# Kernel tuning notes

Measured on AMD Instinct MI355X. Metric: run time of the kernel, lower is better.

The kernel has to match this reference:

```python
import jax, jax.numpy as jnp
import numpy as np

EPS_STD = 1e-5   # PNA std aggregator epsilon
EPS_GN = 1e-5    # GraphNorm epsilon


def setup_inputs() -> dict:
    key = jax.random.key(0)
    B, N, C = 8, 256, 128
    ks = jax.random.split(key, 8)
    w = lambda k, sh: jax.random.normal(k, sh, jnp.float32) * 0.05
    return {
        "x": jax.random.normal(ks[0], (B, N, C), jnp.float32),
        "edge": jax.random.normal(ks[1], (B, N * N, C), jnp.float32),
        "W_edge": w(ks[2], (C, C)), "b_edge": jnp.zeros((C,), jnp.float32),
        "W_pre": w(ks[3], (3 * C, C)), "b_pre": jnp.zeros((C,), jnp.float32),
        "W_post": w(ks[4], (5 * C, C)), "b_post": jnp.zeros((C,), jnp.float32),
        "W_lin": w(ks[5], (C, C)), "b_lin": jnp.zeros((C,), jnp.float32),
        "gn_weight": jnp.ones((C,), jnp.float32),
        "gn_bias": jnp.zeros((C,), jnp.float32),
        "gn_alpha": jnp.ones((C,), jnp.float32),
    }


def reference(x, edge, W_edge, b_edge, W_pre, b_pre, W_post, b_post,
              W_lin, b_lin, gn_weight, gn_bias, gn_alpha):
    B, N, C = x.shape
    res = x
    # edge e = i*N + j: source j -> target i  => reshape to [B, i(target), j(source), C]
    e = edge.reshape(B, N, N, C)
    e_enc = e @ W_edge + b_edge                               # edge_encoder
    x_i = jnp.broadcast_to(x[:, :, None, :], (B, N, N, C))    # target feats
    x_j = jnp.broadcast_to(x[:, None, :, :], (B, N, N, C))    # source feats
    h = jnp.concatenate([x_i, x_j, e_enc], axis=-1)           # [B,N,N,3C]
    m = h @ W_pre + b_pre                                     # pre-MLP messages [B,N,N,C]
    # PNA aggregators over source axis j (graph is fully connected, degree == N)
    mean = m.mean(axis=2)
    mn = m.min(axis=2)
    mx = m.max(axis=2)
    var = (m * m).mean(axis=2) - mean * mean
    std = jnp.sqrt(jax.nn.relu(var) + EPS_STD)
    agg = jnp.concatenate([mean, mn, mx, std], axis=-1)       # [B,N,4C]
    out = jnp.concatenate([x, agg], axis=-1) @ W_post + b_post  # post-MLP [B,N,C]
    out = out @ W_lin + b_lin                                  # final linear
    # GraphNorm with batch=None in the original: stats over ALL B*N nodes
    flat = out.reshape(B * N, C)
    mu = flat.mean(axis=0, keepdims=True)
    centered = flat - gn_alpha * mu
    v = (centered * centered).mean(axis=0, keepdims=True)
    normed = gn_weight * centered / jnp.sqrt(v + EPS_GN) + gn_bias
    y = jax.nn.relu(normed).reshape(B, N, C)
    return y + res
```

## Files before the change

### kernel.cpp

```cpp
#include <hip/hip_runtime.h>
#include <hip/hip_bf16.h>
#include <stdint.h>

typedef __attribute__((ext_vector_type(8))) short bf16x8;
typedef __attribute__((ext_vector_type(4))) float f32x4;
typedef __attribute__((ext_vector_type(4))) unsigned int u32x4;

#define NB 256
#define CC 128

typedef const __attribute__((address_space(1))) void* gvp;
typedef __attribute__((address_space(3))) void* lvp;
#define GLOAD_LDS16(GP, LP) \
  __builtin_amdgcn_global_load_lds((gvp)(uintptr_t)(GP), (lvp)(uintptr_t)(LP), 16, 0, 0)

static __device__ __forceinline__ unsigned int cvt_pk_bf16(float lo, float hi) {
  unsigned int r;
  asm("v_cvt_pk_bf16_f32 %0, %1, %2" : "=v"(r) : "v"(lo), "v"(hi));
  return r;
}
static __device__ __forceinline__ uint16_t f2bf(float f) {
  unsigned u = __builtin_bit_cast(unsigned, f);
  return (uint16_t)((u + 0x7FFFu + ((u >> 16) & 1u)) >> 16);
}

__global__ void k_prep(const float* __restrict__ W_edge, const float* __restrict__ b_edge,
                       const float* __restrict__ W_pre, const float* __restrict__ b_pre,
                       const float* __restrict__ x,
                       uint16_t* __restrict__ wct, float* __restrict__ bc2,
                       float* __restrict__ At, float* __restrict__ Bv) {
  const int c = threadIdx.x;
  if (blockIdx.x < 128) {
    const int k = blockIdx.x;
    float acc = 0.f;
    for (int q = 0; q < CC; ++q)
      acc += W_edge[k * CC + q] * W_pre[(2 * CC + q) * CC + c];
    wct[c * CC + k] = f2bf(acc);
    if (k == 0) {
      float a2 = b_pre[c];
      for (int q = 0; q < CC; ++q) a2 += b_edge[q] * W_pre[(2 * CC + q) * CC + c];
      bc2[c] = a2;
    }
  } else {
    const int m0 = (blockIdx.x - 128) * 2;
    __shared__ float xs[2][CC];
    xs[0][c] = x[(size_t)m0 * CC + c];
    xs[1][c] = x[(size_t)(m0 + 1) * CC + c];
    __syncthreads();
    float a0 = 0.f, a1 = 0.f, v0 = 0.f, v1 = 0.f;
#pragma unroll 4
    for (int k = 0; k < CC; ++k) {
      const float w1 = W_pre[k * CC + c];
      const float w2 = W_pre[(CC + k) * CC + c];
      a0 += xs[0][k] * w1; a1 += xs[1][k] * w1;
      v0 += xs[0][k] * w2; v1 += xs[1][k] * w2;
    }
    At[(size_t)m0 * CC + c] = a0;       At[(size_t)(m0 + 1) * CC + c] = a1;
    Bv[(size_t)m0 * CC + c] = v0;       Bv[(size_t)(m0 + 1) * CC + c] = v1;
  }
}

__global__ __launch_bounds__(256, 4) void k_edge(
    const float* __restrict__ edge, const uint16_t* __restrict__ wct,
    const float* __restrict__ Bv, const float* __restrict__ At,
    const float* __restrict__ bc2, float* __restrict__ agg) {
  __shared__ __align__(16) float ebuf[3][2048];
  __shared__ __align__(16) float bvbuf[2][2048];

  const int blk  = blockIdx.x;
  const int b    = blk >> 8;
  const int tid  = threadIdx.x;
  const int lane = tid & 63;
  const int wv   = tid >> 6;
  const int g    = lane >> 4;
  const int lr   = lane & 15;
  const int cb   = wv * 32;

  bf16x8 bfr[2][4];
#pragma unroll
  for (int t = 0; t < 2; ++t) {
    const uint16_t* p1 = wct + (cb + t * 16 + lr) * CC + g * 8;
#pragma unroll
    for (int ks = 0; ks < 4; ++ks)
      bfr[t][ks] = *(const bf16x8*)(p1 + ks * 32);
  }
  asm volatile("s_waitcnt vmcnt(0)" ::: "memory");

  const uint32_t L0 = wv * 2048 + lane * 16;
  const uint32_t L1 = L0 + 1024;
  const uint32_t S0 = L0 ^ (((L0 >> 9) & 7) << 4);
  const uint32_t S1 = L1 ^ (((L1 >> 9) & 7) << 4);

  const char* egbase  = (const char*)(edge + (size_t)blk * (NB * CC));
  const char* bvgbase = (const char*)(Bv + (size_t)b * (NB * CC));

  auto STAGE_E = [&](int buf, int t) {
    const char* eg = egbase + (size_t)t * 8192;
    char* el = (char*)&ebuf[buf][0];
    GLOAD_LDS16(eg + S0, el + wv * 2048);
    GLOAD_LDS16(eg + S1, el + wv * 2048 + 1024);
  };
  auto STAGE_BV = [&](int buf, int t) {
    const char* bg = bvgbase + (size_t)t * 8192;
    char* bl = (char*)&bvbuf[buf][0];
    GLOAD_LDS16(bg + S0, bl + wv * 2048);
    GLOAD_LDS16(bg + S1, bl + wv * 2048 + 1024);
  };

  float sum0 = 0.f, sum1 = 0.f, ssq0 = 0.f, ssq1 = 0.f;
  float mn0 = 1e30f, mn1 = 1e30f, mx0 = -1e30f, mx1 = -1e30f;
  const int swz = (lr & 7) << 4;

  auto COMPUTE = [&](int ebi, int bvi) {
    const char* eb = (const char*)&ebuf[ebi][0] + lr * 512;
    const char* bb = (const char*)&bvbuf[bvi][0];
    f32x4 acc0 = {0.f, 0.f, 0.f, 0.f}, acc1 = {0.f, 0.f, 0.f, 0.f};
#pragma unroll
    for (int ks = 0; ks < 4; ++ks) {
      const int off = g * 32 + ks * 128;
      f32x4 lo = *(const f32x4*)(eb + (off ^ swz));
      f32x4 hi = *(const f32x4*)(eb + ((off + 16) ^ swz));
      u32x4 aw;
      aw.x = cvt_pk_bf16(lo.x, lo.y);
      aw.y = cvt_pk_bf16(lo.z, lo.w);
      aw.z = cvt_pk_bf16(hi.x, hi.y);
      aw.w = cvt_pk_bf16(hi.z, hi.w);
      bf16x8 af = __builtin_bit_cast(bf16x8, aw);
      acc0 = __builtin_amdgcn_mfma_f32_16x16x32_bf16(af, bfr[0][ks], acc0, 0, 0, 0);
      acc1 = __builtin_amdgcn_mfma_f32_16x16x32_bf16(af, bfr[1][ks], acc1, 0, 0, 0);
    }
#pragma unroll
    for (int r = 0; r < 4; ++r) {
      const int row = g * 4 + r;
      const int sw = (row & 7) << 4;
      const int lin0 = row * 512 + (cb + lr) * 4;
      const float bv0 = *(const float*)(bb + (lin0 ^ sw));
      const float bv1 = *(const float*)(bb + ((lin0 + 64) ^ sw));
      float s0 = acc0[r] + bv0;
      float s1 = acc1[r] + bv1;
      sum0 += s0; ssq0 = fmaf(s0, s0, ssq0);
      mn0 = fminf(mn0, s0); mx0 = fmaxf(mx0, s0);
      sum1 += s1; ssq1 = fmaf(s1, s1, ssq1);
      mn1 = fminf(mn1, s1); mx1 = fmaxf(mx1, s1);
    }
  };

  STAGE_E(0, 0); STAGE_BV(0, 0); STAGE_E(1, 1);

  int eu = 0;
  int bu = 0;
#pragma unroll 1
  for (int t = 0; t < 14; ++t) {
    asm volatile("s_waitcnt vmcnt(2)" ::: "memory");
    __builtin_amdgcn_s_barrier();
    __builtin_amdgcn_sched_barrier(0);
    int esb = eu - 1; if (esb < 0) esb = 2;
    STAGE_BV(bu ^ 1, t + 1);
    STAGE_E(esb, t + 2);
    __builtin_amdgcn_sched_barrier(0);
    COMPUTE(eu, bu);
    eu = (eu == 2) ? 0 : eu + 1;
    bu ^= 1;
  }
  asm volatile("s_waitcnt vmcnt(2)" ::: "memory");
  __builtin_amdgcn_s_barrier();
  __builtin_amdgcn_sched_barrier(0);
  STAGE_BV(1, 15);
  __builtin_amdgcn_sched_barrier(0);
  COMPUTE(2, 0);
  asm volatile("s_waitcnt vmcnt(0)" ::: "memory");
  __builtin_amdgcn_s_barrier();
  __builtin_amdgcn_sched_barrier(0);
  COMPUTE(0, 1);

#pragma unroll
  for (int m = 16; m <= 32; m <<= 1) {
    sum0 += __shfl_xor(sum0, m); ssq0 += __shfl_xor(ssq0, m);
    mn0 = fminf(mn0, __shfl_xor(mn0, m)); mx0 = fmaxf(mx0, __shfl_xor(mx0, m));
    sum1 += __shfl_xor(sum1, m); ssq1 += __shfl_xor(ssq1, m);
    mn1 = fminf(mn1, __shfl_xor(mn1, m)); mx1 = fmaxf(mx1, __shfl_xor(mx1, m));
  }
  if (g == 0) {
#pragma unroll
    for (int t = 0; t < 2; ++t) {
      const int col = cb + t * 16 + lr;
      const float s   = t ? sum1 : sum0;
      const float q   = t ? ssq1 : ssq0;
      const float mnv = t ? mn1 : mn0;
      const float mxv = t ? mx1 : mx0;
      const float tt = At[blk * CC + col] + bc2[col];
      const float mean = s * (1.f / NB);
      const float var = q * (1.f / NB) - mean * mean;
      const float sd = sqrtf(fmaxf(var, 0.f) + 1e-5f);
      float* ap = agg + (size_t)blk * (4 * CC) + col;
      ap[0]      = tt + mean;
      ap[CC]     = tt + mnv;
      ap[2 * CC] = tt + mxv;
      ap[3 * CC] = sd;
    }
  }
}

__global__ __launch_bounds__(256) void k_post(
    const float* __restrict__ x, const float* __restrict__ agg,
    const float* __restrict__ W_post, const float* __restrict__ b_post,
    const float* __restrict__ W_lin, const float* __restrict__ b_lin,
    float* __restrict__ outl, float* __restrict__ psum, float* __restrict__ psq) {
  __shared__ float hx[4][5 * CC];
  __shared__ float o1[4][CC];
  __shared__ float pl[4][CC];
  const int blk = blockIdx.x;
  const int t = threadIdx.x;
  const int row0 = blk * 4;

  for (int idx = t; idx < 4 * 5 * CC; idx += 256) {
    int r = idx / (5 * CC), col = idx - r * (5 * CC);
    hx[r][col] = (col < CC) ? x[(size_t)(row0 + r) * CC + col]
                            : agg[(size_t)(row0 + r) * (4 * CC) + (col - CC)];
  }
  __syncthreads();

  const int c = t & (CC - 1);
  const int rh = t >> 7;
  float acc[2] = {b_post[c], b_post[c]};
  for (int k = 0; k < 5 * CC; k += 4) {
    float w0 = W_post[(k + 0) * CC + c];
    float w1 = W_post[(k + 1) * CC + c];
    float w2 = W_post[(k + 2) * CC + c];
    float w3 = W_post[(k + 3) * CC + c];
#pragma unroll
    for (int i = 0; i < 2; ++i) {
      const f32x4 h4 = *(const f32x4*)&hx[2 * i + rh][k];
      acc[i] += h4.x * w0 + h4.y * w1 + h4.z * w2 + h4.w * w3;
    }
  }
#pragma unroll
  for (int i = 0; i < 2; ++i) o1[2 * i + rh][c] = acc[i];
  __syncthreads();

  float a2[2] = {b_lin[c], b_lin[c]};
  for (int k = 0; k < CC; k += 4) {
    float w0 = W_lin[(k + 0) * CC + c];
    float w1 = W_lin[(k + 1) * CC + c];
    float w2 = W_lin[(k + 2) * CC + c];
    float w3 = W_lin[(k + 3) * CC + c];
#pragma unroll
    for (int i = 0; i < 2; ++i) {
      const f32x4 h4 = *(const f32x4*)&o1[2 * i + rh][k];
      a2[i] += h4.x * w0 + h4.y * w1 + h4.z * w2 + h4.w * w3;
    }
  }
  float ps = 0.f, pq = 0.f;
#pragma unroll
  for (int i = 0; i < 2; ++i) {
    outl[(size_t)(row0 + 2 * i + rh) * CC + c] = a2[i];
    ps += a2[i]; pq += a2[i] * a2[i];
  }
  pl[rh][c] = ps; pl[2 + rh][c] = pq;
  __syncthreads();
  if (t < CC) {
    psum[blk * CC + t] = pl[0][t] + pl[1][t];
    psq[blk * CC + t]  = pl[2][t] + pl[3][t];
  }
}

__global__ __launch_bounds__(256) void k_apply(
    const float* __restrict__ psum, const float* __restrict__ psq,
    const float* __restrict__ outl, const float* __restrict__ x,
    const float* __restrict__ gw, const float* __restrict__ gb,
    const float* __restrict__ alpha, float* __restrict__ y) {
  __shared__ float red[4][CC];
  __shared__ float smu[CC], siv[CC];
  const int t = threadIdx.x;
  const int c = t & (CC - 1);
  const int h = t >> 7;
  float s = 0.f, q = 0.f;
#pragma unroll 4
  for (int i = 0; i < 256; ++i) {
    const int r = h * 256 + i;
    s += psum[r * CC + c];
    q += psq[r * CC + c];
  }
  red[h][c] = s; red[2 + h][c] = q;
  __syncthreads();
  if (t < CC) {
    const float ss = red[0][t] + red[1][t];
    const float qq = red[2][t] + red[3][t];
    const float mu = ss * (1.f / 2048.f);
    const float ex2 = qq * (1.f / 2048.f);
    const float amu = alpha[t] * mu;
    const float v = ex2 - 2.f * amu * mu + amu * amu;
    smu[t] = amu;
    siv[t] = gw[t] / sqrtf(v + 1e-5f);
  }
  __syncthreads();
  const int row0 = blockIdx.x * 8;
#pragma unroll
  for (int r = 0; r < 8; r += 2) {
    const int idx = (row0 + r + h) * CC + c;
    const float o = outl[idx];
    const float val = (o - smu[c]) * siv[c] + gb[c];
    y[idx] = fmaxf(val, 0.f) + x[idx];
  }
}

extern "C" void kernel_launch(void* const* d_in, const int* in_sizes, int n_in,
                              void* d_out, int out_size, void* d_ws, size_t ws_size,
                              hipStream_t stream) {
  const float* x      = (const float*)d_in[0];
  const float* edge   = (const float*)d_in[1];
  const float* W_edge = (const float*)d_in[2];
  const float* b_edge = (const float*)d_in[3];
  const float* W_pre  = (const float*)d_in[4];
  const float* b_pre  = (const float*)d_in[5];
  const float* W_post = (const float*)d_in[6];
  const float* b_post = (const float*)d_in[7];
  const float* W_lin  = (const float*)d_in[8];
  const float* b_lin  = (const float*)d_in[9];
  const float* gw     = (const float*)d_in[10];
  const float* gb     = (const float*)d_in[11];
  const float* alpha  = (const float*)d_in[12];
  float* y = (float*)d_out;

  float* wsf = (float*)d_ws;
  float* bc2   = wsf;
  float* At    = wsf + 128;
  float* Bv    = wsf + 262272;
  float* agg   = wsf + 524416;
  float* outl  = wsf + 1572992;
  float* psum  = wsf + 1835136;
  float* psq   = wsf + 1900672;
  uint16_t* wct = (uint16_t*)(wsf + 1966208);

  k_prep<<<1152, 128, 0, stream>>>(W_edge, b_edge, W_pre, b_pre, x, wct, bc2, At, Bv);
  k_edge<<<2048, 256, 0, stream>>>(edge, wct, Bv, At, bc2, agg);
  k_post<<<512, 256, 0, stream>>>(x, agg, W_post, b_post, W_lin, b_lin, outl, psum, psq);
  k_apply<<<256, 256, 0, stream>>>(psum, psq, outl, x, gw, gb, alpha, y);
}
```

Measured before the change: 107.8 us.

## Stage edge tiles via registers as bf16 in LDS and pack Bv to bf16

The direct global-to-LDS async copies of fp32 edge tiles are replaced by register loads. Each tile is converted to bf16 once and written into padded, double-buffered LDS, so the MFMA A-fragments are read directly as bf16. The per-source Bv term is precomputed as packed bf16 pairs in an MFMA-friendly column order, which halves its global and LDS traffic. The aim is to cut LDS footprint and bandwidth and the redundant per-wave bf16 conversion. In exchange it adds a register round trip, extra barriers per tile, and bf16 rounding of Bv.

```diff
diff --git a/kernel.cpp b/kernel.cpp
--- a/kernel.cpp
+++ b/kernel.cpp
@@ -8,11 +8,6 @@
 
 #define NB 256
 #define CC 128
-
-typedef const __attribute__((address_space(1))) void* gvp;
-typedef __attribute__((address_space(3))) void* lvp;
-#define GLOAD_LDS16(GP, LP) \
-  __builtin_amdgcn_global_load_lds((gvp)(uintptr_t)(GP), (lvp)(uintptr_t)(LP), 16, 0, 0)
 
 static __device__ __forceinline__ unsigned int cvt_pk_bf16(float lo, float hi) {
   unsigned int r;
@@ -28,7 +23,7 @@
                        const float* __restrict__ W_pre, const float* __restrict__ b_pre,
                        const float* __restrict__ x,
                        uint16_t* __restrict__ wct, float* __restrict__ bc2,
-                       float* __restrict__ At, float* __restrict__ Bv) {
+                       float* __restrict__ At, unsigned* __restrict__ bvl) {
   const int c = threadIdx.x;
   if (blockIdx.x < 128) {
     const int k = blockIdx.x;
@@ -56,16 +51,22 @@
       v0 += xs[0][k] * w2; v1 += xs[1][k] * w2;
     }
     At[(size_t)m0 * CC + c] = a0;       At[(size_t)(m0 + 1) * CC + c] = a1;
-    Bv[(size_t)m0 * CC + c] = v0;       Bv[(size_t)(m0 + 1) * CC + c] = v1;
+    const float p0 = __shfl_down(v0, 16);
+    const float p1 = __shfl_down(v1, 16);
+    if ((c & 31) < 16) {
+      const int di = (c >> 5) * 16 + (c & 15);
+      bvl[(size_t)m0 * 64 + di]       = ((unsigned)f2bf(p0) << 16) | f2bf(v0);
+      bvl[(size_t)(m0 + 1) * 64 + di] = ((unsigned)f2bf(p1) << 16) | f2bf(v1);
+    }
   }
 }
 
 __global__ __launch_bounds__(256, 4) void k_edge(
     const float* __restrict__ edge, const uint16_t* __restrict__ wct,
-    const float* __restrict__ Bv, const float* __restrict__ At,
+    const unsigned* __restrict__ bvl, const float* __restrict__ At,
     const float* __restrict__ bc2, float* __restrict__ agg) {
-  __shared__ __align__(16) float ebuf[3][2048];
-  __shared__ __align__(16) float bvbuf[2][2048];
+  __shared__ __align__(16) char ebuf[2][16 * 272];
+  __shared__ __align__(16) char bvbuf[2][16 * 272];
 
   const int blk  = blockIdx.x;
   const int b    = blk >> 8;
@@ -86,56 +87,49 @@
   }
   asm volatile("s_waitcnt vmcnt(0)" ::: "memory");
 
-  const uint32_t L0 = wv * 2048 + lane * 16;
-  const uint32_t L1 = L0 + 1024;
-  const uint32_t S0 = L0 ^ (((L0 >> 9) & 7) << 4);
-  const uint32_t S1 = L1 ^ (((L1 >> 9) & 7) << 4);
-
   const char* egbase  = (const char*)(edge + (size_t)blk * (NB * CC));
-  const char* bvgbase = (const char*)(Bv + (size_t)b * (NB * CC));
-
-  auto STAGE_E = [&](int buf, int t) {
-    const char* eg = egbase + (size_t)t * 8192;
-    char* el = (char*)&ebuf[buf][0];
-    GLOAD_LDS16(eg + S0, el + wv * 2048);
-    GLOAD_LDS16(eg + S1, el + wv * 2048 + 1024);
+  const char* bvgbase = (const char*)(bvl + (size_t)b * (NB * 64));
+  const int sdst = (tid >> 4) * 272 + (tid & 15) * 16;
+
+  f32x4 eA0, eA1, eB0, eB1;
+  u32x4 vA, vB;
+
+  auto LOADA = [&](int t) {
+    const f32x4* s = (const f32x4*)(egbase + (size_t)t * 8192 + tid * 32);
+    eA0 = s[0]; eA1 = s[1];
+    vA = *(const u32x4*)(bvgbase + (size_t)t * 4096 + tid * 16);
   };
-  auto STAGE_BV = [&](int buf, int t) {
-    const char* bg = bvgbase + (size_t)t * 8192;
-    char* bl = (char*)&bvbuf[buf][0];
-    GLOAD_LDS16(bg + S0, bl + wv * 2048);
-    GLOAD_LDS16(bg + S1, bl + wv * 2048 + 1024);
+  auto LOADB = [&](int t) {
+    const f32x4* s = (const f32x4*)(egbase + (size_t)t * 8192 + tid * 32);
+    eB0 = s[0]; eB1 = s[1];
+    vB = *(const u32x4*)(bvgbase + (size_t)t * 4096 + tid * 16);
+  };
+  auto STORE = [&](char* eb_, char* bb_, const f32x4& e0, const f32x4& e1, const u32x4& v) {
+    u32x4 w;
+    w.x = cvt_pk_bf16(e0.x, e0.y); w.y = cvt_pk_bf16(e0.z, e0.w);
+    w.z = cvt_pk_bf16(e1.x, e1.y); w.w = cvt_pk_bf16(e1.z, e1.w);
+    *(u32x4*)(eb_ + sdst) = w;
+    *(u32x4*)(bb_ + sdst) = v;
   };
 
   float sum0 = 0.f, sum1 = 0.f, ssq0 = 0.f, ssq1 = 0.f;
   float mn0 = 1e30f, mn1 = 1e30f, mx0 = -1e30f, mx1 = -1e30f;
-  const int swz = (lr & 7) << 4;
-
-  auto COMPUTE = [&](int ebi, int bvi) {
-    const char* eb = (const char*)&ebuf[ebi][0] + lr * 512;
-    const char* bb = (const char*)&bvbuf[bvi][0];
+
+  auto COMPUTE = [&](const char* eb_, const char* bb_) {
+    const char* eb = eb_ + lr * 272;
     f32x4 acc0 = {0.f, 0.f, 0.f, 0.f}, acc1 = {0.f, 0.f, 0.f, 0.f};
 #pragma unroll
     for (int ks = 0; ks < 4; ++ks) {
-      const int off = g * 32 + ks * 128;
-      f32x4 lo = *(const f32x4*)(eb + (off ^ swz));
-      f32x4 hi = *(const f32x4*)(eb + ((off + 16) ^ swz));
-      u32x4 aw;
-      aw.x = cvt_pk_bf16(lo.x, lo.y);
-      aw.y = cvt_pk_bf16(lo.z, lo.w);
-      aw.z = cvt_pk_bf16(hi.x, hi.y);
-      aw.w = cvt_pk_bf16(hi.z, hi.w);
-      bf16x8 af = __builtin_bit_cast(bf16x8, aw);
+      bf16x8 af = *(const bf16x8*)(eb + g * 16 + ks * 64);
       acc0 = __builtin_amdgcn_mfma_f32_16x16x32_bf16(af, bfr[0][ks], acc0, 0, 0, 0);
       acc1 = __builtin_amdgcn_mfma_f32_16x16x32_bf16(af, bfr[1][ks], acc1, 0, 0, 0);
     }
 #pragma unroll
     for (int r = 0; r < 4; ++r) {
       const int row = g * 4 + r;
-      const int sw = (row & 7) << 4;
-      const int lin0 = row * 512 + (cb + lr) * 4;
-      const float bv0 = *(const float*)(bb + (lin0 ^ sw));
-      const float bv1 = *(const float*)(bb + ((lin0 + 64) ^ sw));
+      const unsigned pv = *(const unsigned*)(bb_ + row * 272 + wv * 64 + lr * 4);
+      const float bv0 = __builtin_bit_cast(float, pv << 16);
+      const float bv1 = __builtin_bit_cast(float, pv & 0xffff0000u);
       float s0 = acc0[r] + bv0;
       float s1 = acc1[r] + bv1;
       sum0 += s0; ssq0 = fmaf(s0, s0, ssq0);
@@ -145,33 +139,33 @@
     }
   };
 
-  STAGE_E(0, 0); STAGE_BV(0, 0); STAGE_E(1, 1);
-
-  int eu = 0;
-  int bu = 0;
+  LOADA(0); LOADB(1);
+  __builtin_amdgcn_sched_barrier(0);
+
 #pragma unroll 1
-  for (int t = 0; t < 14; ++t) {
-    asm volatile("s_waitcnt vmcnt(2)" ::: "memory");
+  for (int tt = 0; tt < 16; tt += 2) {
     __builtin_amdgcn_s_barrier();
-    __builtin_amdgcn_sched_barrier(0);
-    int esb = eu - 1; if (esb < 0) esb = 2;
-    STAGE_BV(bu ^ 1, t + 1);
-    STAGE_E(esb, t + 2);
-    __builtin_amdgcn_sched_barrier(0);
-    COMPUTE(eu, bu);
-    eu = (eu == 2) ? 0 : eu + 1;
-    bu ^= 1;
-  }
-  asm volatile("s_waitcnt vmcnt(2)" ::: "memory");
-  __builtin_amdgcn_s_barrier();
-  __builtin_amdgcn_sched_barrier(0);
-  STAGE_BV(1, 15);
-  __builtin_amdgcn_sched_barrier(0);
-  COMPUTE(2, 0);
-  asm volatile("s_waitcnt vmcnt(0)" ::: "memory");
-  __builtin_amdgcn_s_barrier();
-  __builtin_amdgcn_sched_barrier(0);
-  COMPUTE(0, 1);
+    asm volatile("s_waitcnt vmcnt(3)" ::: "memory");
+    __builtin_amdgcn_sched_barrier(0);
+    STORE(ebuf[0], bvbuf[0], eA0, eA1, vA);
+    asm volatile("s_waitcnt lgkmcnt(0)" ::: "memory");
+    __builtin_amdgcn_sched_barrier(0);
+    __builtin_amdgcn_s_barrier();
+    if (tt + 2 < 16) LOADA(tt + 2);
+    __builtin_amdgcn_sched_barrier(0);
+    COMPUTE(ebuf[0], bvbuf[0]);
+    __builtin_amdgcn_s_barrier();
+    if (tt < 14) { asm volatile("s_waitcnt vmcnt(3)" ::: "memory"); }
+    else         { asm volatile("s_waitcnt vmcnt(0)" ::: "memory"); }
+    __builtin_amdgcn_sched_barrier(0);
+    STORE(ebuf[1], bvbuf[1], eB0, eB1, vB);
+    asm volatile("s_waitcnt lgkmcnt(0)" ::: "memory");
+    __builtin_amdgcn_sched_barrier(0);
+    __builtin_amdgcn_s_barrier();
+    if (tt + 3 < 16) LOADB(tt + 3);
+    __builtin_amdgcn_sched_barrier(0);
+    COMPUTE(ebuf[1], bvbuf[1]);
+  }
 
 #pragma unroll
   for (int m = 16; m <= 32; m <<= 1) {
@@ -188,14 +182,14 @@
       const float q   = t ? ssq1 : ssq0;
       const float mnv = t ? mn1 : mn0;
       const float mxv = t ? mx1 : mx0;
-      const float tt = At[blk * CC + col] + bc2[col];
+      const float tt2 = At[blk * CC + col] + bc2[col];
       const float mean = s * (1.f / NB);
       const float var = q * (1.f / NB) - mean * mean;
       const float sd = sqrtf(fmaxf(var, 0.f) + 1e-5f);
       float* ap = agg + (size_t)blk * (4 * CC) + col;
-      ap[0]      = tt + mean;
-      ap[CC]     = tt + mnv;
-      ap[2 * CC] = tt + mxv;
+      ap[0]      = tt2 + mean;
+      ap[CC]     = tt2 + mnv;
+      ap[2 * CC] = tt2 + mxv;
       ap[3 * CC] = sd;
     }
   }
@@ -325,15 +319,15 @@
   float* wsf = (float*)d_ws;
   float* bc2   = wsf;
   float* At    = wsf + 128;
-  float* Bv    = wsf + 262272;
-  float* agg   = wsf + 524416;
-  float* outl  = wsf + 1572992;
-  float* psum  = wsf + 1835136;
-  float* psq   = wsf + 1900672;
-  uint16_t* wct = (uint16_t*)(wsf + 1966208);
-
-  k_prep<<<1152, 128, 0, stream>>>(W_edge, b_edge, W_pre, b_pre, x, wct, bc2, At, Bv);
-  k_edge<<<2048, 256, 0, stream>>>(edge, wct, Bv, At, bc2, agg);
+  float* agg   = wsf + 262272;
+  float* outl  = wsf + 1310848;
+  float* psum  = wsf + 1572992;
+  float* psq   = wsf + 1638528;
+  uint16_t* wct = (uint16_t*)(wsf + 1704064);
+  unsigned* bvl = (unsigned*)(wsf + 1712256);
+
+  k_prep<<<1152, 128, 0, stream>>>(W_edge, b_edge, W_pre, b_pre, x, wct, bc2, At, bvl);
+  k_edge<<<2048, 256, 0, stream>>>(edge, wct, bvl, At, bc2, agg);
   k_post<<<512, 256, 0, stream>>>(x, agg, W_post, b_post, W_lin, b_lin, outl, psum, psq);
   k_apply<<<256, 256, 0, stream>>>(psum, psq, outl, x, gw, gb, alpha, y);
 }
```

Result: no change. 106.7 us (-1.1%).
